# Performance work log

Hardware: AMD Instinct MI355X
Metric: run time of the kernel (lower is better)

## Reference

```python
import jax, jax.numpy as jnp
import numpy as np

HEAD_SIZE = 64
EMBED = 1024


def setup_inputs() -> dict:
    key = jax.random.key(0)
    k1, k2, k3, k4 = jax.random.split(key, 4)
    B, T, D = 4, 4096, EMBED
    x = jax.random.normal(k1, (B, T, D), dtype=jnp.float32)
    # nn.Linear weights: [out_features, in_features]
    Wk = jax.random.normal(k2, (HEAD_SIZE, D), dtype=jnp.float32) * (D ** -0.5)
    Wq = jax.random.normal(k3, (HEAD_SIZE, D), dtype=jnp.float32) * (D ** -0.5)
    Wv = jax.random.normal(k4, (D, D), dtype=jnp.float32) * (D ** -0.5)
    return {"x": x, "Wk": Wk, "Wq": Wq, "Wv": Wv}


def reference(x, Wk, Wq, Wv):
    # x: [B, T, D]
    B, T, D = x.shape
    K = jnp.einsum('btd,hd->bth', x, Wk)      # [B, T, H]
    Q = jnp.einsum('btd,hd->bth', x, Wq)      # [B, T, H]
    V = jnp.einsum('btd,ed->bte', x, Wv)      # [B, T, D]
    scale = 1.0 / jnp.sqrt(jnp.float32(HEAD_SIZE))
    scores = jnp.einsum('bth,bsh->bts', Q, K) * scale  # [B, T, T]
    causal = jnp.tril(jnp.ones((T, T), dtype=bool))
    scores = jnp.where(causal, scores, jnp.float32(-jnp.inf))
    attn = jax.nn.softmax(scores, axis=-1)
    out = jnp.einsum('bts,bse->bte', attn, V)  # [B, T, D]
    return out
```

## Files before the change

### kernel.cpp

```cpp
#include <hip/hip_runtime.h>
#include <hip/hip_bf16.h>


typedef __attribute__((ext_vector_type(8))) short bf16x8;
typedef __attribute__((ext_vector_type(4))) float f32x4;

typedef unsigned short u16;
typedef unsigned int u32;

__device__ inline u16 f2bf(float f) {
    u32 u = __builtin_bit_cast(u32, f);
    u = (u + 0x7fff + ((u >> 16) & 1)) >> 16;
    return (u16)u;
}

__device__ inline u32 pkbf(float a, float b) {
    return (u32)f2bf(a) | ((u32)f2bf(b) << 16);
}

__device__ inline void g2lds16(const void* g, void* l) {
    __builtin_amdgcn_global_load_lds(
        (const __attribute__((address_space(1))) unsigned int*)g,
        (__attribute__((address_space(3))) unsigned int*)l, 16, 0, 0);
}


__global__ void cvt_x(const float* __restrict__ src, u16* __restrict__ dst,
                      int n) {
    const int i = (blockIdx.x * blockDim.x + threadIdx.x) * 4;
    if (i + 3 < n) {
        const float4 v = *(const float4*)(src + i);
        dst[i + 0] = f2bf(v.x);
        dst[i + 1] = f2bf(v.y);
        dst[i + 2] = f2bf(v.z);
        dst[i + 3] = f2bf(v.w);
    }
}

__global__ void cvt_w(const float* __restrict__ Wk, const float* __restrict__ Wq,
                      const float* __restrict__ Wv,
                      u16* __restrict__ Wkb, u16* __restrict__ Wqb,
                      u16* __restrict__ Wvb, float qscale) {
    const int i = (blockIdx.x * blockDim.x + threadIdx.x) * 4;
    const float* src; u16* dst; int j; float s = 1.0f;
    if (i < 65536)        { src = Wk; dst = Wkb; j = i; }
    else if (i < 131072)  { src = Wq; dst = Wqb; j = i - 65536; s = qscale; }
    else                  { src = Wv; dst = Wvb; j = i - 131072; }
    const float4 v = *(const float4*)(src + j);
    dst[j + 0] = f2bf(v.x * s);
    dst[j + 1] = f2bf(v.y * s);
    dst[j + 2] = f2bf(v.z * s);
    dst[j + 3] = f2bf(v.w * s);
}

template <int MODE>
__device__ __forceinline__ void gemm_body(
    int m0, int n0,
    const u16* __restrict__ A,
    const u16* __restrict__ B0, const u16* __restrict__ B1, int nsplit,
    u16* __restrict__ D0, u16* __restrict__ D1,
    u16* Alds, u16* Blds)
{
    const int tid  = threadIdx.x;
    const int lane = tid & 63, w = tid >> 6;
    const int quad = lane >> 4, l15 = lane & 15;
    const int wr = w >> 1, wc = w & 1;
    const int mrow0 = wr * 64, ncol0 = wc * 64;

    f32x4 acc[4][4] = {};

    const int srow = (lane >> 3);
    const int scol = (lane & 7) * 8;

    for (int k0 = 0; k0 < 1024; k0 += 64) {
        __syncthreads();
#pragma unroll
        for (int c = 0; c < 4; ++c) {
            const int chunk = c * 4 + w;
            const int row = chunk * 8 + srow;
            const u16* ga = A + (size_t)(m0 + row) * 1024 + k0 + scol;
            g2lds16(ga, &Alds[chunk * 512]);
            const int brow = n0 + row;
            const u16* gb = (brow < nsplit ? B0 + (size_t)brow * 1024
                                           : B1 + (size_t)(brow - nsplit) * 1024)
                            + k0 + scol;
            g2lds16(gb, &Blds[chunk * 512]);
        }
        __syncthreads();

#pragma unroll
        for (int kk = 0; kk < 64; kk += 32) {
            bf16x8 af[4], bfr[4];
#pragma unroll
            for (int mb = 0; mb < 4; ++mb)
                af[mb] = *(const bf16x8*)&Alds[(mrow0 + mb * 16 + l15) * 64 + kk + quad * 8];
#pragma unroll
            for (int nb = 0; nb < 4; ++nb)
                bfr[nb] = *(const bf16x8*)&Blds[(ncol0 + nb * 16 + l15) * 64 + kk + quad * 8];
#pragma unroll
            for (int mb = 0; mb < 4; ++mb)
#pragma unroll
                for (int nb = 0; nb < 4; ++nb)
                    acc[mb][nb] = __builtin_amdgcn_mfma_f32_16x16x32_bf16(
                        af[mb], bfr[nb], acc[mb][nb], 0, 0, 0);
        }
    }

#pragma unroll
    for (int mb = 0; mb < 4; ++mb)
#pragma unroll
        for (int nb = 0; nb < 4; ++nb)
#pragma unroll
            for (int r = 0; r < 4; ++r) {
                const int row = m0 + mrow0 + mb * 16 + quad * 4 + r;
                const int col = n0 + ncol0 + nb * 16 + l15;
                const u16 v = f2bf(acc[mb][nb][r]);
                if (MODE == 1) {
                    const int h = col & 63;
                    u16* dst = (col < 64) ? D0 : D1;
                    const size_t idx = (size_t)((row >> 4) * 2 + (h >> 5)) * 512
                                     + ((row & 15) + ((h >> 3) & 3) * 16) * 8
                                     + (h & 7);
                    dst[idx] = v;
                } else {
                    const size_t idx = (size_t)((row >> 4) * 512 + (col >> 5)) * 512
                                     + ((row & 15) + ((col >> 3) & 3) * 16) * 8
                                     + (col & 7);
                    D0[idx] = v;
                }
            }
}

__global__ __launch_bounds__(256, 2) void gemm_all(
    const u16* __restrict__ xb,
    const u16* __restrict__ Wqb, const u16* __restrict__ Wkb,
    const u16* __restrict__ Wvb,
    u16* __restrict__ Qf, u16* __restrict__ Kf, u16* __restrict__ Vf)
{
    __shared__ u16 Alds[128 * 64];
    __shared__ u16 Blds[128 * 64];
    const int d = blockIdx.x;
    if (d < 128) {
        gemm_body<1>(d * 128, 0, xb, Wqb, Wkb, 64, Qf, Kf, Alds, Blds);
    } else {
        const int dd = d - 128;
        gemm_body<2>((dd >> 7) * 128, (dd & 127) * 128, Wvb, xb, xb, 1 << 30,
                     Vf, nullptr, Alds, Blds);
    }
}

__global__ __launch_bounds__(512, 4) void attn_fa(
    const u16* __restrict__ Qf,
    const u16* __restrict__ Kf,
    const u16* __restrict__ Vf,
    float* __restrict__ Out)
{
    __shared__ u16 Vlds[2][16 * 512];
    __shared__ u16 Plds[2][128 * 40];

    const int tid  = threadIdx.x;
    const int lane = tid & 63, w = tid >> 6;
    const int quad = lane >> 4, l15 = lane & 15;

    const int d  = blockIdx.y * 128 + blockIdx.x;
    const int g  = d >> 4;
    const int qt = (g < 16) ? (31 - g) : (g - 16);
    const int e0 = ((d >> 2) & 3) * 256;
    const int b  = d & 3;
    const int bt0 = b * 4096;

    const int qs = w >> 1, es = w & 1;
    const int qrow0 = qt * 128 + qs * 32;

    bf16x8 qf[2][2];
#pragma unroll
    for (int mb = 0; mb < 2; ++mb)
#pragma unroll
        for (int kk = 0; kk < 2; ++kk) {
            const int btile = (bt0 + qrow0 + mb * 16) >> 4;
            qf[mb][kk] = *(const bf16x8*)&Qf[(size_t)(btile * 2 + kk) * 512 + lane * 8];
        }

    const short o = (short)0x3F80;
    const bf16x8 ones = {o, o, o, o, o, o, o, o};

    f32x4 acc[2][8] = {};
    f32x4 accl[2]  = {};

    const int ntiles = 4 * qt + 4;
    const int qlim = qrow0 + 31;

    auto stageV = [&](int buf, int it) {
        const int stile = (bt0 + it * 32) >> 5;
#pragma unroll
        for (int t2 = 0; t2 < 2; ++t2) {
            const int t = w * 2 + t2;
            g2lds16(&Vf[(size_t)(((e0 >> 4) + t) * 512 + stile) * 512 + lane * 8],
                    &Vlds[buf][t * 512]);
        }
    };

    auto loadK = [&](int jt, bf16x8* kf) {
#pragma unroll
        for (int kk = 0; kk < 2; ++kk) {
            const int kt = ((bt0 + jt * 32 + es * 16) >> 4) * 2 + kk;
            kf[kk] = *(const bf16x8*)&Kf[(size_t)kt * 512 + lane * 8];
        }
    };

    auto computeP = [&](int jt, const bf16x8* kf) {
        const int s0 = jt * 32;
        f32x4 sf[2] = {};
#pragma unroll
        for (int mb = 0; mb < 2; ++mb)
#pragma unroll
            for (int kk = 0; kk < 2; ++kk)
                sf[mb] = __builtin_amdgcn_mfma_f32_16x16x32_bf16(
                    qf[mb][kk], kf[kk], sf[mb], 0, 0, 0);
        if (s0 + 31 > qrow0) {
            const int colabs = s0 + es * 16 + l15;
#pragma unroll
            for (int mb = 0; mb < 2; ++mb)
#pragma unroll
                for (int r = 0; r < 4; ++r) {
                    const int rowabs = qrow0 + mb * 16 + quad * 4 + r;
                    sf[mb][r] = (colabs <= rowabs) ? sf[mb][r] : -__builtin_inff();
                }
        }
        u16* Pl = &Plds[jt & 1][(qs * 32 + quad * 4) * 40 + es * 16 + l15];
#pragma unroll
        for (int mb = 0; mb < 2; ++mb) {
            const u32 p01 = pkbf(exp2f(sf[mb][0]), exp2f(sf[mb][1]));
            const u32 p23 = pkbf(exp2f(sf[mb][2]), exp2f(sf[mb][3]));
            u16* base = Pl + mb * 16 * 40;
            base[0]      = (u16)p01;
            base[40]     = (u16)(p01 >> 16);
            base[80]     = (u16)p23;
            base[120]    = (u16)(p23 >> 16);
        }
    };

    stageV(0, 0);
    {
        bf16x8 kf0[2];
        loadK(0, kf0);
        computeP(0, kf0);
    }

    for (int it = 0; it < ntiles; ++it) {
        __syncthreads();
        const int buf = it & 1;
        const bool haveNext = (it + 1 < ntiles);
        const bool nextActive = haveNext && ((it + 1) * 32 <= qlim);
        const bool curActive = (it * 32 <= qlim);

        if (haveNext) stageV(buf ^ 1, it + 1);
        bf16x8 kf[2];
        if (nextActive) loadK(it + 1, kf);

        if (curActive) {
            bf16x8 pf[2];
#pragma unroll
            for (int mb = 0; mb < 2; ++mb)
                pf[mb] = *(const bf16x8*)&Plds[buf][(qs * 32 + mb * 16 + l15) * 40 + quad * 8];
#pragma unroll
            for (int mb = 0; mb < 2; ++mb)
                accl[mb] = __builtin_amdgcn_mfma_f32_16x16x32_bf16(
                    pf[mb], ones, accl[mb], 0, 0, 0);
#pragma unroll
            for (int nb = 0; nb < 8; ++nb) {
                bf16x8 vf = *(const bf16x8*)&Vlds[buf][(es * 8 + nb) * 512 + lane * 8];
#pragma unroll
                for (int mb = 0; mb < 2; ++mb)
                    acc[mb][nb] = __builtin_amdgcn_mfma_f32_16x16x32_bf16(
                        pf[mb], vf, acc[mb][nb], 0, 0, 0);
            }
        }

        if (nextActive) computeP(it + 1, kf);
    }

    float rl[2][4];
#pragma unroll
    for (int mb = 0; mb < 2; ++mb)
#pragma unroll
        for (int r = 0; r < 4; ++r) rl[mb][r] = 1.0f / accl[mb][r];
#pragma unroll
    for (int mb = 0; mb < 2; ++mb)
#pragma unroll
        for (int nb = 0; nb < 8; ++nb)
#pragma unroll
            for (int r = 0; r < 4; ++r) {
                const int row = qrow0 + mb * 16 + quad * 4 + r;
                const int col = e0 + es * 128 + nb * 16 + l15;
                Out[(size_t)(bt0 + row) * 1024 + col] = acc[mb][nb][r] * rl[mb][r];
            }
}

extern "C" void kernel_launch(void* const* d_in, const int* in_sizes, int n_in,
                              void* d_out, int out_size, void* d_ws, size_t ws_size,
                              hipStream_t stream) {
    const float* x  = (const float*)d_in[0];
    const float* Wk = (const float*)d_in[1];
    const float* Wq = (const float*)d_in[2];
    const float* Wv = (const float*)d_in[3];

    const int nx  = in_sizes[0];
    const int nwk = in_sizes[1];
    const int nwq = in_sizes[2];
    const int nwv = in_sizes[3];

    u16* xb  = (u16*)d_ws;
    u16* Wkb = xb  + (size_t)nx;
    u16* Wqb = Wkb + (size_t)nwk;
    u16* Wvb = Wqb + (size_t)nwq;
    u16* Qf  = Wvb + (size_t)nwv;
    u16* Kf  = Qf  + (size_t)1024 * 2 * 512;
    u16* Vf  = Kf  + (size_t)1024 * 2 * 512;
    float* out = (float*)d_out;

    const float qscale = 0.125f * 1.44269504088896f;

    cvt_x<<<nx / 1024, 256, 0, stream>>>(x, xb, nx);
    cvt_w<<<(nwk + nwq + nwv) / 1024, 256, 0, stream>>>(Wk, Wq, Wv,
                                                        Wkb, Wqb, Wvb, qscale);

    gemm_all<<<1152, 256, 0, stream>>>(xb, Wqb, Wkb, Wvb, Qf, Kf, Vf);

    attn_fa<<<dim3(128, 4), 512, 0, stream>>>(Qf, Kf, Vf, out);
}
```

Measured before the change: 351.6 us.

## Retile attention to 4-wave blocks with 64x64 warp tiles over 128 columns

Each attention block now has 256 threads and covers 128 query rows by 128 output columns, where before it had 512 threads covering 256 columns. Each wave computes a 64x64 tile instead of 32x128, and the grid doubles to 1024 blocks with a new interleaved causal load-balancing order. Q fragments are reloaded from global memory inside computeP instead of being kept in registers. The per-wave tile is meant to reuse P and V better. In exchange, each block recomputes QK^T for its own column slice, and both the QK work and the Q reads increase.

Measured after the change: 528.8 us. 1.5x slower.

```diff
diff --git a/kernel.cpp b/kernel.cpp
--- a/kernel.cpp
+++ b/kernel.cpp
@@ -12,10 +12,6 @@
     u32 u = __builtin_bit_cast(u32, f);
     u = (u + 0x7fff + ((u >> 16) & 1)) >> 16;
     return (u16)u;
-}
-
-__device__ inline u32 pkbf(float a, float b) {
-    return (u32)f2bf(a) | ((u32)f2bf(b) << 16);
 }
 
 __device__ inline void g2lds16(const void* g, void* l) {
@@ -149,53 +145,45 @@
     }
 }
 
-__global__ __launch_bounds__(512, 4) void attn_fa(
+__global__ __launch_bounds__(256, 4) void attn_fa(
     const u16* __restrict__ Qf,
     const u16* __restrict__ Kf,
     const u16* __restrict__ Vf,
     float* __restrict__ Out)
 {
-    __shared__ u16 Vlds[2][16 * 512];
+    __shared__ u16 Vlds[2][8 * 512];
     __shared__ u16 Plds[2][128 * 40];
 
     const int tid  = threadIdx.x;
     const int lane = tid & 63, w = tid >> 6;
     const int quad = lane >> 4, l15 = lane & 15;
 
-    const int d  = blockIdx.y * 128 + blockIdx.x;
-    const int g  = d >> 4;
-    const int qt = (g < 16) ? (31 - g) : (g - 16);
-    const int e0 = ((d >> 2) & 3) * 256;
+    const int d  = blockIdx.x;
     const int b  = d & 3;
+    const int e0 = (d >> 2) & 7;
+    const int g  = d >> 5;
+    const int h  = g & 7, j = g >> 3;
+    const int qt = (j == 0) ? h : (j == 1) ? 31 - h : (j == 2) ? 15 - h : 16 + h;
     const int bt0 = b * 4096;
 
-    const int qs = w >> 1, es = w & 1;
-    const int qrow0 = qt * 128 + qs * 32;
-
-    bf16x8 qf[2][2];
-#pragma unroll
-    for (int mb = 0; mb < 2; ++mb)
-#pragma unroll
-        for (int kk = 0; kk < 2; ++kk) {
-            const int btile = (bt0 + qrow0 + mb * 16) >> 4;
-            qf[mb][kk] = *(const bf16x8*)&Qf[(size_t)(btile * 2 + kk) * 512 + lane * 8];
-        }
+    const int wr = w >> 1, wc = w & 1;
+    const int qm0 = qt * 128 + wr * 64;
+    const int slim = qm0 + 63;
 
     const short o = (short)0x3F80;
     const bf16x8 ones = {o, o, o, o, o, o, o, o};
 
-    f32x4 acc[2][8] = {};
-    f32x4 accl[2]  = {};
+    f32x4 acc[4][4] = {};
+    f32x4 accl[4] = {};
 
     const int ntiles = 4 * qt + 4;
-    const int qlim = qrow0 + 31;
 
     auto stageV = [&](int buf, int it) {
         const int stile = (bt0 + it * 32) >> 5;
 #pragma unroll
         for (int t2 = 0; t2 < 2; ++t2) {
             const int t = w * 2 + t2;
-            g2lds16(&Vf[(size_t)(((e0 >> 4) + t) * 512 + stile) * 512 + lane * 8],
+            g2lds16(&Vf[(size_t)((e0 * 8 + t) * 512 + stile) * 512 + lane * 8],
                     &Vlds[buf][t * 512]);
         }
     };
@@ -203,41 +191,40 @@
     auto loadK = [&](int jt, bf16x8* kf) {
 #pragma unroll
         for (int kk = 0; kk < 2; ++kk) {
-            const int kt = ((bt0 + jt * 32 + es * 16) >> 4) * 2 + kk;
+            const int kt = ((bt0 + jt * 32 + wc * 16) >> 4) * 2 + kk;
             kf[kk] = *(const bf16x8*)&Kf[(size_t)kt * 512 + lane * 8];
         }
     };
 
     auto computeP = [&](int jt, const bf16x8* kf) {
         const int s0 = jt * 32;
-        f32x4 sf[2] = {};
-#pragma unroll
-        for (int mb = 0; mb < 2; ++mb)
-#pragma unroll
-            for (int kk = 0; kk < 2; ++kk)
+        f32x4 sf[4] = {};
+#pragma unroll
+        for (int mb = 0; mb < 4; ++mb) {
+            const int btile = (bt0 + qm0 + mb * 16) >> 4;
+#pragma unroll
+            for (int kk = 0; kk < 2; ++kk) {
+                const bf16x8 q = *(const bf16x8*)&Qf[(size_t)(btile * 2 + kk) * 512 + lane * 8];
                 sf[mb] = __builtin_amdgcn_mfma_f32_16x16x32_bf16(
-                    qf[mb][kk], kf[kk], sf[mb], 0, 0, 0);
-        if (s0 + 31 > qrow0) {
-            const int colabs = s0 + es * 16 + l15;
-#pragma unroll
-            for (int mb = 0; mb < 2; ++mb)
+                    q, kf[kk], sf[mb], 0, 0, 0);
+            }
+        }
+        if (s0 + wc * 16 + 15 > qm0) {
+            const int colabs = s0 + wc * 16 + l15;
+#pragma unroll
+            for (int mb = 0; mb < 4; ++mb)
 #pragma unroll
                 for (int r = 0; r < 4; ++r) {
-                    const int rowabs = qrow0 + mb * 16 + quad * 4 + r;
+                    const int rowabs = qm0 + mb * 16 + quad * 4 + r;
                     sf[mb][r] = (colabs <= rowabs) ? sf[mb][r] : -__builtin_inff();
                 }
         }
-        u16* Pl = &Plds[jt & 1][(qs * 32 + quad * 4) * 40 + es * 16 + l15];
-#pragma unroll
-        for (int mb = 0; mb < 2; ++mb) {
-            const u32 p01 = pkbf(exp2f(sf[mb][0]), exp2f(sf[mb][1]));
-            const u32 p23 = pkbf(exp2f(sf[mb][2]), exp2f(sf[mb][3]));
-            u16* base = Pl + mb * 16 * 40;
-            base[0]      = (u16)p01;
-            base[40]     = (u16)(p01 >> 16);
-            base[80]     = (u16)p23;
-            base[120]    = (u16)(p23 >> 16);
-        }
+        u16* Pl = &Plds[jt & 1][(wr * 64 + quad * 4) * 40 + wc * 16 + l15];
+#pragma unroll
+        for (int mb = 0; mb < 4; ++mb)
+#pragma unroll
+            for (int r = 0; r < 4; ++r)
+                Pl[(mb * 16 + r) * 40] = f2bf(exp2f(sf[mb][r]));
     };
 
     stageV(0, 0);
@@ -251,50 +238,49 @@
         __syncthreads();
         const int buf = it & 1;
         const bool haveNext = (it + 1 < ntiles);
-        const bool nextActive = haveNext && ((it + 1) * 32 <= qlim);
-        const bool curActive = (it * 32 <= qlim);
+        const bool nextAct = haveNext && ((it + 1) * 32 <= slim);
+        const bool curAct  = (it * 32 <= slim);
 
         if (haveNext) stageV(buf ^ 1, it + 1);
         bf16x8 kf[2];
-        if (nextActive) loadK(it + 1, kf);
-
-        if (curActive) {
-            bf16x8 pf[2];
-#pragma unroll
-            for (int mb = 0; mb < 2; ++mb)
-                pf[mb] = *(const bf16x8*)&Plds[buf][(qs * 32 + mb * 16 + l15) * 40 + quad * 8];
-#pragma unroll
-            for (int mb = 0; mb < 2; ++mb)
+        if (nextAct) loadK(it + 1, kf);
+
+        if (curAct) {
+            bf16x8 pf[4];
+#pragma unroll
+            for (int mb = 0; mb < 4; ++mb)
+                pf[mb] = *(const bf16x8*)&Plds[buf][(wr * 64 + mb * 16 + l15) * 40 + quad * 8];
+#pragma unroll
+            for (int mb = 0; mb < 4; ++mb)
                 accl[mb] = __builtin_amdgcn_mfma_f32_16x16x32_bf16(
                     pf[mb], ones, accl[mb], 0, 0, 0);
 #pragma unroll
-            for (int nb = 0; nb < 8; ++nb) {
-                bf16x8 vf = *(const bf16x8*)&Vlds[buf][(es * 8 + nb) * 512 + lane * 8];
-#pragma unroll
-                for (int mb = 0; mb < 2; ++mb)
+            for (int nb = 0; nb < 4; ++nb) {
+                const bf16x8 vf = *(const bf16x8*)&Vlds[buf][(wc * 4 + nb) * 512 + lane * 8];
+#pragma unroll
+                for (int mb = 0; mb < 4; ++mb)
                     acc[mb][nb] = __builtin_amdgcn_mfma_f32_16x16x32_bf16(
                         pf[mb], vf, acc[mb][nb], 0, 0, 0);
             }
         }
 
-        if (nextActive) computeP(it + 1, kf);
-    }
-
-    float rl[2][4];
-#pragma unroll
-    for (int mb = 0; mb < 2; ++mb)
-#pragma unroll
-        for (int r = 0; r < 4; ++r) rl[mb][r] = 1.0f / accl[mb][r];
-#pragma unroll
-    for (int mb = 0; mb < 2; ++mb)
-#pragma unroll
-        for (int nb = 0; nb < 8; ++nb)
+        if (nextAct) computeP(it + 1, kf);
+    }
+
+#pragma unroll
+    for (int mb = 0; mb < 4; ++mb) {
+        float rl[4];
+#pragma unroll
+        for (int r = 0; r < 4; ++r) rl[r] = 1.0f / accl[mb][r];
+#pragma unroll
+        for (int nb = 0; nb < 4; ++nb)
 #pragma unroll
             for (int r = 0; r < 4; ++r) {
-                const int row = qrow0 + mb * 16 + quad * 4 + r;
-                const int col = e0 + es * 128 + nb * 16 + l15;
-                Out[(size_t)(bt0 + row) * 1024 + col] = acc[mb][nb][r] * rl[mb][r];
+                const int row = qm0 + mb * 16 + quad * 4 + r;
+                const int col = e0 * 128 + wc * 64 + nb * 16 + l15;
+                Out[(size_t)(bt0 + row) * 1024 + col] = acc[mb][nb][r] * rl[r];
             }
+    }
 }
 
 extern "C" void kernel_launch(void* const* d_in, const int* in_sizes, int n_in,
@@ -327,5 +313,5 @@
 
     gemm_all<<<1152, 256, 0, stream>>>(xb, Wqb, Wkb, Wvb, Qf, Kf, Vf);
 
-    attn_fa<<<dim3(128, 4), 512, 0, stream>>>(Qf, Kf, Vf, out);
-}
+    attn_fa<<<1024, 256, 0, stream>>>(Qf, Kf, Vf, out);
+}
```
